# Kernel tuning notes

Hardware: AMD Instinct MI355X
Metric: run time of the kernel (lower is better)

The kernel has to match this reference:

```python
import jax, jax.numpy as jnp
import numpy as np

N_NODES = 50000
N_EDGES = 800000
D_IN = 128
D_HID = 128
D_OUT = 128


def _gcn_layer(x, W, b, src, dst, norm):
    # dense projection then edge-weighted gather -> scatter-add at dst
    h = x @ W                                   # [N, d_out]
    msg = h[src] * norm[:, None]                # [E, d_out]
    out = jax.ops.segment_sum(msg, dst, num_segments=N_NODES)
    return out + b


def setup_inputs() -> dict:
    key = jax.random.key(0)
    k = jax.random.split(key, 8)
    x = jax.random.normal(k[0], (N_NODES, D_IN), dtype=jnp.float32)
    edge_index = jax.random.randint(k[1], (2, N_EDGES), 0, N_NODES, dtype=jnp.int64)
    edge_weight = jax.random.uniform(k[2], (N_EDGES,), dtype=jnp.float32)
    # GCNConv params (glorot-ish scale)
    s1 = 1.0 / np.sqrt(D_IN)
    s2 = 1.0 / np.sqrt(D_HID)
    W1 = jax.random.normal(k[3], (D_IN, D_HID), dtype=jnp.float32) * s1
    b1 = jnp.zeros((D_HID,), dtype=jnp.float32)
    W2 = jax.random.normal(k[4], (D_HID, D_OUT), dtype=jnp.float32) * s2
    b2 = jnp.zeros((D_OUT,), dtype=jnp.float32)
    return {"x": x, "edge_index": edge_index, "edge_weight": edge_weight,
            "W1": W1, "b1": b1, "W2": W2, "b2": b2}


def reference(x, edge_index, edge_weight, W1, b1, W2, b2):
    src, dst = edge_index[0], edge_index[1]
    # gcn_norm (add_self_loops=False): deg from scatter-add of edge_weight at dst
    deg = jax.ops.segment_sum(edge_weight, dst, num_segments=N_NODES)
    dinv = jnp.where(deg > 0, jax.lax.rsqrt(jnp.maximum(deg, 1e-30)), 0.0)
    norm = dinv[src] * edge_weight * dinv[dst]  # [E]
    h = jax.nn.relu(_gcn_layer(x, W1, b1, src, dst, norm))
    out = _gcn_layer(h, W2, b2, src, dst, norm)
    # F.dropout in eval mode (deterministic reference) is identity
    return out
```

## Files before the change

kernel.cpp:

```cpp
#include <hip/hip_runtime.h>

#define N_NODES 50000
#define N_EDGES 800000
#define D 128
#define MAXDEG 64
#define NBUCK 196
#define BUCKCAP 5120
#define EPB 4096
#define NBB 196
#define GB 782
#define SP 136

typedef __attribute__((ext_vector_type(8))) short bf16x8;
typedef __attribute__((ext_vector_type(4))) float f32x4;

__device__ inline unsigned short f2bf(float f) {
    unsigned u = __float_as_uint(f);
    unsigned r = (u + 0x7fffu + ((u >> 16) & 1u)) >> 16;
    return (unsigned short)r;
}

__global__ __launch_bounds__(256) void k_bucket(const int* __restrict__ src,
                                                const int* __restrict__ dst,
                                                const float* __restrict__ ew,
                                                int* __restrict__ cursor,
                                                uint2* __restrict__ buck,
                                                const float* __restrict__ W1,
                                                const float* __restrict__ W2,
                                                unsigned short* __restrict__ Wt1,
                                                unsigned short* __restrict__ Wt2) {
    if (blockIdx.x >= NBB) {
        const float* W = (blockIdx.x == NBB) ? W1 : W2;
        unsigned short* Wt = (blockIdx.x == NBB) ? Wt1 : Wt2;
        for (int idx = threadIdx.x; idx < D * D; idx += 256) {
            int n = idx & 127, k = idx >> 7;
            Wt[n * D + k] = f2bf(W[k * D + n]);
        }
        return;
    }
    __shared__ uint2 sorted[EPB];
    __shared__ int hist[NBUCK];
    __shared__ int scn[NBUCK];
    __shared__ int gbase[NBUCK];
    __shared__ int s[256];
    int tid = threadIdx.x;
    int e0 = blockIdx.x * EPB;
    for (int i = tid; i < NBUCK; i += 256) hist[i] = 0;
    __syncthreads();
    #pragma unroll
    for (int j = 0; j < 16; ++j) {
        int e = e0 + j * 256 + tid;
        if (e < N_EDGES) atomicAdd(&hist[dst[e] >> 8], 1);
    }
    __syncthreads();
    int v = tid < NBUCK ? hist[tid] : 0;
    s[tid] = v;
    __syncthreads();
    for (int off = 1; off < 256; off <<= 1) {
        int u = tid >= off ? s[tid - off] : 0;
        __syncthreads();
        s[tid] += u;
        __syncthreads();
    }
    int excl = s[tid] - v;
    if (tid < NBUCK) {
        scn[tid] = excl;
        gbase[tid] = v ? atomicAdd(&cursor[tid], v) : 0;
        hist[tid] = excl;
    }
    __syncthreads();
    #pragma unroll
    for (int j = 0; j < 16; ++j) {
        int e = e0 + j * 256 + tid;
        if (e < N_EDGES) {
            int d = dst[e];
            int sv = src[e];
            unsigned wf = min(__float2uint_rn(ew[e] * 65536.f), 65535u);
            int slot = atomicAdd(&hist[d >> 8], 1);
            sorted[slot] = make_uint2(((unsigned)sv << 16) | wf, (unsigned)d);
        }
    }
    __syncthreads();
    int total = min(EPB, N_EDGES - e0);
    for (int i = tid; i < total; i += 256) {
        uint2 en = sorted[i];
        int bk = (int)(en.y >> 8);
        int g = gbase[bk] + (i - scn[bk]);
        if (g < BUCKCAP)
            buck[(size_t)bk * BUCKCAP + g] = make_uint2(en.x, en.y & 255u);
    }
}

__global__ __launch_bounds__(256) void k_build_gemm(
        const int* __restrict__ cursor, const uint2* __restrict__ buck,
        unsigned* __restrict__ csr, int* __restrict__ cnt,
        float* __restrict__ dinv,
        const float* __restrict__ X, const unsigned short* __restrict__ Wt1,
        unsigned short* __restrict__ h0) {
    __shared__ union SM {
        struct {
            unsigned csr_loc[256 * MAXDEG];
            int cnt_loc[256];
            int deg_loc[256];
        } b;
        unsigned short sX[64 * D];
    } sm;
    int tid = threadIdx.x;

    if (blockIdx.x < NBUCK) {
        int b = blockIdx.x;
        sm.b.cnt_loc[tid] = 0;
        sm.b.deg_loc[tid] = 0;
        {
            uint4* z4 = (uint4*)sm.b.csr_loc;
            #pragma unroll
            for (int i = 0; i < (256 * MAXDEG / 4) / 256; ++i)
                z4[i * 256 + tid] = make_uint4(0u, 0u, 0u, 0u);
        }
        __syncthreads();
        int n = min(cursor[b], BUCKCAP);
        const uint2* bb = buck + (size_t)b * BUCKCAP;
        for (int i = tid; i < n; i += 256) {
            uint2 e = bb[i];
            int ln = e.y;
            int slot = atomicAdd(&sm.b.cnt_loc[ln], 1);
            if (slot < MAXDEG) sm.b.csr_loc[ln * MAXDEG + slot] = e.x;
            atomicAdd(&sm.b.deg_loc[ln], (int)(e.x & 0xffffu));
        }
        __syncthreads();
        int node0 = b * 256;
        int nnodes = min(256, N_NODES - node0);
        uint4* g = (uint4*)(csr + (size_t)node0 * MAXDEG);
        const uint4* l = (const uint4*)sm.b.csr_loc;
        int nv = nnodes * (MAXDEG / 4);
        for (int i = tid; i < nv; i += 256) g[i] = l[i];
        if (tid < nnodes) {
            int node = node0 + tid;
            cnt[node] = min(sm.b.cnt_loc[tid], MAXDEG);
            float sum = (float)sm.b.deg_loc[tid] * (1.f / 65536.f);
            dinv[node] = sum > 0.f ? rsqrtf(fmaxf(sum, 1e-30f)) : 0.f;
        }
        return;
    }

    int row0 = (blockIdx.x - NBUCK) * 64;
    int nr = min(64, N_NODES - row0);
    {
        const float4* xs = (const float4*)(X + (size_t)row0 * D);
        int nvec = nr * (D / 4);
        for (int i = tid; i < nvec; i += 256) {
            float4 v = xs[i];
            ushort4 o;
            o.x = f2bf(v.x); o.y = f2bf(v.y); o.z = f2bf(v.z); o.w = f2bf(v.w);
            *(ushort4*)(sm.sX + i * 4) = o;
        }
    }
    __syncthreads();

    int wave = tid >> 6, lane = tid & 63;
    int m = lane & 15, quad = lane >> 4;
    f32x4 acc[8];
    #pragma unroll
    for (int i = 0; i < 8; ++i) acc[i] = (f32x4){0.f, 0.f, 0.f, 0.f};

    const unsigned short* aBase = sm.sX + (wave * 16 + m) * D + quad * 8;
    #pragma unroll
    for (int c = 0; c < 4; ++c) {
        bf16x8 a = *(const bf16x8*)(aBase + c * 32);
        #pragma unroll
        for (int n0 = 0; n0 < 8; ++n0) {
            bf16x8 b = *(const bf16x8*)(Wt1 + (n0 * 16 + m) * D + c * 32 + quad * 8);
            acc[n0] = __builtin_amdgcn_mfma_f32_16x16x32_bf16(a, b, acc[n0], 0, 0, 0);
        }
    }

    unsigned short* sOut = sm.sX + wave * 16 * D;
    __syncthreads();
    #pragma unroll
    for (int n0 = 0; n0 < 8; ++n0)
        #pragma unroll
        for (int i = 0; i < 4; ++i)
            sOut[(quad * 4 + i) * D + n0 * 16 + m] = f2bf(acc[n0][i]);
    __syncthreads();
    int rr = lane >> 2, c0 = (lane & 3) * 32;
    int grow = row0 + wave * 16 + rr;
    if (grow < N_NODES) {
        uint4* dstp = (uint4*)(h0 + (size_t)grow * D + c0);
        const uint4* srcp = (const uint4*)(sOut + rr * D + c0);
        dstp[0] = srcp[0]; dstp[1] = srcp[1]; dstp[2] = srcp[2]; dstp[3] = srcp[3];
    }
}

__global__ __launch_bounds__(256) void k_agg_mm(const unsigned short* __restrict__ H,
                                                const int* __restrict__ cnt,
                                                const unsigned* __restrict__ csr,
                                                const float* __restrict__ dinv,
                                                const float* __restrict__ b1,
                                                const unsigned short* __restrict__ Wt2,
                                                unsigned short* __restrict__ Hb) {
    __shared__ unsigned short sT[16 * SP];
    int tid = threadIdx.x, wave = tid >> 6, lane = tid & 63;
    int g = lane >> 4, fl = lane & 15;
    int nb = blockIdx.x * 16;
    int node = nb + wave * 4 + g;

    int end = min(cnt[node], MAXDEG);
    const uint4* row4 = (const uint4*)(csr + (size_t)node * MAXDEG);
    float acc[8] = {0.f, 0.f, 0.f, 0.f, 0.f, 0.f, 0.f, 0.f};
    for (int b0 = 0; b0 < end; b0 += 16) {
        int r0 = b0 >> 2;
        uint4 c0 = row4[r0], c1 = row4[r0 + 1], c2 = row4[r0 + 2], c3 = row4[r0 + 3];
        unsigned cs[16] = {c0.x, c0.y, c0.z, c0.w, c1.x, c1.y, c1.z, c1.w,
                           c2.x, c2.y, c2.z, c2.w, c3.x, c3.y, c3.z, c3.w};
        uint4 u[16];
        float nmv[16];
        #pragma unroll
        for (int j = 0; j < 16; ++j) {
            unsigned sv = cs[j] >> 16;
            u[j] = *(const uint4*)(H + (size_t)sv * D + fl * 8);
            nmv[j] = (float)(cs[j] & 0xffffu) * (1.f / 65536.f) * dinv[sv];
        }
        #pragma unroll
        for (int j = 0; j < 16; ++j) {
            unsigned a0[4] = {u[j].x, u[j].y, u[j].z, u[j].w};
            #pragma unroll
            for (int q = 0; q < 4; ++q) {
                acc[2 * q]     += __uint_as_float(a0[q] << 16) * nmv[j];
                acc[2 * q + 1] += __uint_as_float(a0[q] & 0xffff0000u) * nmv[j];
            }
        }
    }
    {
        float dn = dinv[node];
        int f = fl * 8;
        float4 bv0 = *(const float4*)(b1 + f);
        float4 bv1 = *(const float4*)(b1 + f + 4);
        ushort4 o0, o1;
        o0.x = f2bf(fmaxf(acc[0] * dn + bv0.x, 0.f));
        o0.y = f2bf(fmaxf(acc[1] * dn + bv0.y, 0.f));
        o0.z = f2bf(fmaxf(acc[2] * dn + bv0.z, 0.f));
        o0.w = f2bf(fmaxf(acc[3] * dn + bv0.w, 0.f));
        o1.x = f2bf(fmaxf(acc[4] * dn + bv1.x, 0.f));
        o1.y = f2bf(fmaxf(acc[5] * dn + bv1.y, 0.f));
        o1.z = f2bf(fmaxf(acc[6] * dn + bv1.z, 0.f));
        o1.w = f2bf(fmaxf(acc[7] * dn + bv1.w, 0.f));
        unsigned short* tp = sT + (wave * 4 + g) * SP + f;
        *(ushort4*)(tp) = o0;
        *(ushort4*)(tp + 4) = o1;
    }
    __syncthreads();

    int m = lane & 15, quad = lane >> 4;
    f32x4 acc2[2];
    acc2[0] = (f32x4){0.f, 0.f, 0.f, 0.f};
    acc2[1] = (f32x4){0.f, 0.f, 0.f, 0.f};
    #pragma unroll
    for (int c = 0; c < 4; ++c) {
        bf16x8 a = *(const bf16x8*)(sT + m * SP + c * 32 + quad * 8);
        #pragma unroll
        for (int t = 0; t < 2; ++t) {
            int n0 = wave * 2 + t;
            bf16x8 b = *(const bf16x8*)(Wt2 + (n0 * 16 + m) * D + c * 32 + quad * 8);
            acc2[t] = __builtin_amdgcn_mfma_f32_16x16x32_bf16(a, b, acc2[t], 0, 0, 0);
        }
    }
    float dv[4];
    #pragma unroll
    for (int i = 0; i < 4; ++i) dv[i] = dinv[nb + quad * 4 + i];
    __syncthreads();
    #pragma unroll
    for (int t = 0; t < 2; ++t)
        #pragma unroll
        for (int i = 0; i < 4; ++i)
            sT[(quad * 4 + i) * SP + (wave * 2 + t) * 16 + m] = f2bf(acc2[t][i] * dv[i]);
    __syncthreads();
    int rr = tid >> 4, cc = (tid & 15) * 8;
    *(uint4*)(Hb + (size_t)(nb + rr) * D + cc) = *(const uint4*)(sT + rr * SP + cc);
}

__global__ __launch_bounds__(256) void k_aggregate(const unsigned short* __restrict__ H,
                                                   const int* __restrict__ cnt,
                                                   const unsigned* __restrict__ csr,
                                                   const float* __restrict__ dinv,
                                                   const float* __restrict__ bias,
                                                   float* __restrict__ out) {
    int tid = threadIdx.x, wave = tid >> 6, lane = tid & 63;
    int g = lane >> 4, fl = lane & 15;
    int node = blockIdx.x * 16 + wave * 4 + g;

    int end = min(cnt[node], MAXDEG);
    const uint4* row4 = (const uint4*)(csr + (size_t)node * MAXDEG);
    float acc[8] = {0.f, 0.f, 0.f, 0.f, 0.f, 0.f, 0.f, 0.f};
    for (int b0 = 0; b0 < end; b0 += 16) {
        int r0 = b0 >> 2;
        uint4 c0 = row4[r0], c1 = row4[r0 + 1], c2 = row4[r0 + 2], c3 = row4[r0 + 3];
        unsigned cs[16] = {c0.x, c0.y, c0.z, c0.w, c1.x, c1.y, c1.z, c1.w,
                           c2.x, c2.y, c2.z, c2.w, c3.x, c3.y, c3.z, c3.w};
        uint4 u[16];
        float nmv[16];
        #pragma unroll
        for (int j = 0; j < 16; ++j) {
            unsigned sv = cs[j] >> 16;
            u[j] = *(const uint4*)(H + (size_t)sv * D + fl * 8);
            nmv[j] = (float)(cs[j] & 0xffffu) * (1.f / 65536.f);
        }
        #pragma unroll
        for (int j = 0; j < 16; ++j) {
            unsigned a0[4] = {u[j].x, u[j].y, u[j].z, u[j].w};
            #pragma unroll
            for (int q = 0; q < 4; ++q) {
                acc[2 * q]     += __uint_as_float(a0[q] << 16) * nmv[j];
                acc[2 * q + 1] += __uint_as_float(a0[q] & 0xffff0000u) * nmv[j];
            }
        }
    }
    float dn = dinv[node];
    int f = fl * 8;
    float4 bv0 = *(const float4*)(bias + f);
    float4 bv1 = *(const float4*)(bias + f + 4);
    float* op = out + (size_t)node * D + f;
    *(float4*)(op) = make_float4(acc[0] * dn + bv0.x, acc[1] * dn + bv0.y,
                                 acc[2] * dn + bv0.z, acc[3] * dn + bv0.w);
    *(float4*)(op + 4) = make_float4(acc[4] * dn + bv1.x, acc[5] * dn + bv1.y,
                                     acc[6] * dn + bv1.z, acc[7] * dn + bv1.w);
}

extern "C" void kernel_launch(void* const* d_in, const int* in_sizes, int n_in,
                              void* d_out, int out_size, void* d_ws, size_t ws_size,
                              hipStream_t stream) {
    const float* x   = (const float*)d_in[0];
    const int*   ei  = (const int*)d_in[1];
    const float* ew  = (const float*)d_in[2];
    const float* W1  = (const float*)d_in[3];
    const float* b1  = (const float*)d_in[4];
    const float* W2  = (const float*)d_in[5];
    const float* b2  = (const float*)d_in[6];
    float* out = (float*)d_out;

    const int* src = ei;
    const int* dst = ei + N_EDGES;

    char* base = (char*)d_ws;
    size_t off = 0;
    auto take = [&](size_t bytes) -> char* {
        char* p = base + off;
        off += (bytes + 255) & ~(size_t)255;
        return p;
    };
    int*      cursor = (int*)take(NBUCK * 4);
    size_t zero_bytes = off;
    float*    dinv = (float*)take(N_NODES * 4);
    int*      cnt  = (int*)take(N_NODES * 4);
    uint2*    buck = (uint2*)take((size_t)NBUCK * BUCKCAP * 8);
    unsigned* csr  = (unsigned*)take((size_t)N_NODES * MAXDEG * 4);
    unsigned short* Wt1 = (unsigned short*)take(D * D * 2);
    unsigned short* Wt2 = (unsigned short*)take(D * D * 2);
    unsigned short* h0  = (unsigned short*)take((size_t)N_NODES * D * 2);
    unsigned short* hb  = (unsigned short*)take((size_t)N_NODES * D * 2);

    hipMemsetAsync(d_ws, 0, zero_bytes, stream);

    const int FB = N_NODES / 16;

    k_bucket<<<NBB + 2, 256, 0, stream>>>(src, dst, ew, cursor, buck,
                                          W1, W2, Wt1, Wt2);
    k_build_gemm<<<NBUCK + GB, 256, 0, stream>>>(cursor, buck, csr, cnt, dinv,
                                                 x, Wt1, h0);
    k_agg_mm<<<FB, 256, 0, stream>>>(h0, cnt, csr, dinv, b1, Wt2, hb);
    k_aggregate<<<FB, 256, 0, stream>>>(hb, cnt, csr, dinv, b2, out);
}
```

Baseline: 196.9 us.

## Co-schedule edge bucket sort with first GEMM, split CSR build into own kernel

The weight transpose moves into a tiny separate kernel. The edge bucketing now runs in the same launch as the X·W1 GEMM blocks, and the CSR build becomes its own kernel. The GEMM used to share a launch with the CSR build; it now overlaps the sort instead. This rebalances the work so the large per-block LDS of the CSR build no longer sits with the GEMM blocks, at the cost of one extra kernel launch.

Result: slower. 212.6 us (+7.9%).

```diff
diff --git a/kernel.cpp b/kernel.cpp
--- a/kernel.cpp
+++ b/kernel.cpp
@@ -20,130 +20,87 @@
     return (unsigned short)r;
 }
 
-__global__ __launch_bounds__(256) void k_bucket(const int* __restrict__ src,
-                                                const int* __restrict__ dst,
-                                                const float* __restrict__ ew,
-                                                int* __restrict__ cursor,
-                                                uint2* __restrict__ buck,
-                                                const float* __restrict__ W1,
-                                                const float* __restrict__ W2,
-                                                unsigned short* __restrict__ Wt1,
-                                                unsigned short* __restrict__ Wt2) {
-    if (blockIdx.x >= NBB) {
-        const float* W = (blockIdx.x == NBB) ? W1 : W2;
-        unsigned short* Wt = (blockIdx.x == NBB) ? Wt1 : Wt2;
-        for (int idx = threadIdx.x; idx < D * D; idx += 256) {
-            int n = idx & 127, k = idx >> 7;
-            Wt[n * D + k] = f2bf(W[k * D + n]);
-        }
-        return;
-    }
-    __shared__ uint2 sorted[EPB];
-    __shared__ int hist[NBUCK];
-    __shared__ int scn[NBUCK];
-    __shared__ int gbase[NBUCK];
-    __shared__ int s[256];
-    int tid = threadIdx.x;
-    int e0 = blockIdx.x * EPB;
-    for (int i = tid; i < NBUCK; i += 256) hist[i] = 0;
-    __syncthreads();
-    #pragma unroll
-    for (int j = 0; j < 16; ++j) {
-        int e = e0 + j * 256 + tid;
-        if (e < N_EDGES) atomicAdd(&hist[dst[e] >> 8], 1);
-    }
-    __syncthreads();
-    int v = tid < NBUCK ? hist[tid] : 0;
-    s[tid] = v;
-    __syncthreads();
-    for (int off = 1; off < 256; off <<= 1) {
-        int u = tid >= off ? s[tid - off] : 0;
-        __syncthreads();
-        s[tid] += u;
-        __syncthreads();
-    }
-    int excl = s[tid] - v;
-    if (tid < NBUCK) {
-        scn[tid] = excl;
-        gbase[tid] = v ? atomicAdd(&cursor[tid], v) : 0;
-        hist[tid] = excl;
-    }
-    __syncthreads();
-    #pragma unroll
-    for (int j = 0; j < 16; ++j) {
-        int e = e0 + j * 256 + tid;
-        if (e < N_EDGES) {
-            int d = dst[e];
-            int sv = src[e];
-            unsigned wf = min(__float2uint_rn(ew[e] * 65536.f), 65535u);
-            int slot = atomicAdd(&hist[d >> 8], 1);
-            sorted[slot] = make_uint2(((unsigned)sv << 16) | wf, (unsigned)d);
-        }
-    }
-    __syncthreads();
-    int total = min(EPB, N_EDGES - e0);
-    for (int i = tid; i < total; i += 256) {
-        uint2 en = sorted[i];
-        int bk = (int)(en.y >> 8);
-        int g = gbase[bk] + (i - scn[bk]);
-        if (g < BUCKCAP)
-            buck[(size_t)bk * BUCKCAP + g] = make_uint2(en.x, en.y & 255u);
-    }
-}
-
-__global__ __launch_bounds__(256) void k_build_gemm(
-        const int* __restrict__ cursor, const uint2* __restrict__ buck,
-        unsigned* __restrict__ csr, int* __restrict__ cnt,
-        float* __restrict__ dinv,
+__global__ __launch_bounds__(256) void k_prep(const float* __restrict__ W1,
+                                              const float* __restrict__ W2,
+                                              unsigned short* __restrict__ Wt1,
+                                              unsigned short* __restrict__ Wt2) {
+    const float* W = (blockIdx.x == 0) ? W1 : W2;
+    unsigned short* Wt = (blockIdx.x == 0) ? Wt1 : Wt2;
+    for (int idx = threadIdx.x; idx < D * D; idx += 256) {
+        int n = idx & 127, k = idx >> 7;
+        Wt[n * D + k] = f2bf(W[k * D + n]);
+    }
+}
+
+__global__ __launch_bounds__(256) void k_sort_gemm(
+        const int* __restrict__ src, const int* __restrict__ dst,
+        const float* __restrict__ ew,
+        int* __restrict__ cursor, uint2* __restrict__ buck,
         const float* __restrict__ X, const unsigned short* __restrict__ Wt1,
         unsigned short* __restrict__ h0) {
     __shared__ union SM {
         struct {
-            unsigned csr_loc[256 * MAXDEG];
-            int cnt_loc[256];
-            int deg_loc[256];
-        } b;
+            uint2 sorted[EPB];
+            int hist[NBUCK];
+            int scn[NBUCK];
+            int gbase[NBUCK];
+            int s[256];
+        } so;
         unsigned short sX[64 * D];
     } sm;
     int tid = threadIdx.x;
 
-    if (blockIdx.x < NBUCK) {
-        int b = blockIdx.x;
-        sm.b.cnt_loc[tid] = 0;
-        sm.b.deg_loc[tid] = 0;
-        {
-            uint4* z4 = (uint4*)sm.b.csr_loc;
-            #pragma unroll
-            for (int i = 0; i < (256 * MAXDEG / 4) / 256; ++i)
-                z4[i * 256 + tid] = make_uint4(0u, 0u, 0u, 0u);
-        }
-        __syncthreads();
-        int n = min(cursor[b], BUCKCAP);
-        const uint2* bb = buck + (size_t)b * BUCKCAP;
-        for (int i = tid; i < n; i += 256) {
-            uint2 e = bb[i];
-            int ln = e.y;
-            int slot = atomicAdd(&sm.b.cnt_loc[ln], 1);
-            if (slot < MAXDEG) sm.b.csr_loc[ln * MAXDEG + slot] = e.x;
-            atomicAdd(&sm.b.deg_loc[ln], (int)(e.x & 0xffffu));
-        }
-        __syncthreads();
-        int node0 = b * 256;
-        int nnodes = min(256, N_NODES - node0);
-        uint4* g = (uint4*)(csr + (size_t)node0 * MAXDEG);
-        const uint4* l = (const uint4*)sm.b.csr_loc;
-        int nv = nnodes * (MAXDEG / 4);
-        for (int i = tid; i < nv; i += 256) g[i] = l[i];
-        if (tid < nnodes) {
-            int node = node0 + tid;
-            cnt[node] = min(sm.b.cnt_loc[tid], MAXDEG);
-            float sum = (float)sm.b.deg_loc[tid] * (1.f / 65536.f);
-            dinv[node] = sum > 0.f ? rsqrtf(fmaxf(sum, 1e-30f)) : 0.f;
+    if (blockIdx.x < NBB) {
+        int e0 = blockIdx.x * EPB;
+        for (int i = tid; i < NBUCK; i += 256) sm.so.hist[i] = 0;
+        __syncthreads();
+        #pragma unroll
+        for (int j = 0; j < 16; ++j) {
+            int e = e0 + j * 256 + tid;
+            if (e < N_EDGES) atomicAdd(&sm.so.hist[dst[e] >> 8], 1);
+        }
+        __syncthreads();
+        int v = tid < NBUCK ? sm.so.hist[tid] : 0;
+        sm.so.s[tid] = v;
+        __syncthreads();
+        for (int off = 1; off < 256; off <<= 1) {
+            int u = tid >= off ? sm.so.s[tid - off] : 0;
+            __syncthreads();
+            sm.so.s[tid] += u;
+            __syncthreads();
+        }
+        int excl = sm.so.s[tid] - v;
+        if (tid < NBUCK) {
+            sm.so.scn[tid] = excl;
+            sm.so.gbase[tid] = v ? atomicAdd(&cursor[tid], v) : 0;
+            sm.so.hist[tid] = excl;
+        }
+        __syncthreads();
+        #pragma unroll
+        for (int j = 0; j < 16; ++j) {
+            int e = e0 + j * 256 + tid;
+            if (e < N_EDGES) {
+                int d = dst[e];
+                int sv = src[e];
+                unsigned wf = min(__float2uint_rn(ew[e] * 65536.f), 65535u);
+                int slot = atomicAdd(&sm.so.hist[d >> 8], 1);
+                sm.so.sorted[slot] = make_uint2(((unsigned)sv << 16) | wf,
+                                                (unsigned)d);
+            }
+        }
+        __syncthreads();
+        int total = min(EPB, N_EDGES - e0);
+        for (int i = tid; i < total; i += 256) {
+            uint2 en = sm.so.sorted[i];
+            int bk = (int)(en.y >> 8);
+            int g = sm.so.gbase[bk] + (i - sm.so.scn[bk]);
+            if (g < BUCKCAP)
+                buck[(size_t)bk * BUCKCAP + g] = make_uint2(en.x, en.y & 255u);
         }
         return;
     }
 
-    int row0 = (blockIdx.x - NBUCK) * 64;
+    int row0 = (blockIdx.x - NBB) * 64;
     int nr = min(64, N_NODES - row0);
     {
         const float4* xs = (const float4*)(X + (size_t)row0 * D);
@@ -188,6 +145,48 @@
         uint4* dstp = (uint4*)(h0 + (size_t)grow * D + c0);
         const uint4* srcp = (const uint4*)(sOut + rr * D + c0);
         dstp[0] = srcp[0]; dstp[1] = srcp[1]; dstp[2] = srcp[2]; dstp[3] = srcp[3];
+    }
+}
+
+__global__ __launch_bounds__(256) void k_build(
+        const int* __restrict__ cursor, const uint2* __restrict__ buck,
+        unsigned* __restrict__ csr, int* __restrict__ cnt,
+        float* __restrict__ dinv) {
+    __shared__ unsigned csr_loc[256 * MAXDEG];
+    __shared__ int cnt_loc[256];
+    __shared__ int deg_loc[256];
+    int tid = threadIdx.x;
+    int b = blockIdx.x;
+    cnt_loc[tid] = 0;
+    deg_loc[tid] = 0;
+    {
+        uint4* z4 = (uint4*)csr_loc;
+        #pragma unroll
+        for (int i = 0; i < (256 * MAXDEG / 4) / 256; ++i)
+            z4[i * 256 + tid] = make_uint4(0u, 0u, 0u, 0u);
+    }
+    __syncthreads();
+    int n = min(cursor[b], BUCKCAP);
+    const uint2* bb = buck + (size_t)b * BUCKCAP;
+    for (int i = tid; i < n; i += 256) {
+        uint2 e = bb[i];
+        int ln = e.y;
+        int slot = atomicAdd(&cnt_loc[ln], 1);
+        if (slot < MAXDEG) csr_loc[ln * MAXDEG + slot] = e.x;
+        atomicAdd(&deg_loc[ln], (int)(e.x & 0xffffu));
+    }
+    __syncthreads();
+    int node0 = b * 256;
+    int nnodes = min(256, N_NODES - node0);
+    uint4* g = (uint4*)(csr + (size_t)node0 * MAXDEG);
+    const uint4* l = (const uint4*)csr_loc;
+    int nv = nnodes * (MAXDEG / 4);
+    for (int i = tid; i < nv; i += 256) g[i] = l[i];
+    if (tid < nnodes) {
+        int node = node0 + tid;
+        cnt[node] = min(cnt_loc[tid], MAXDEG);
+        float sum = (float)deg_loc[tid] * (1.f / 65536.f);
+        dinv[node] = sum > 0.f ? rsqrtf(fmaxf(sum, 1e-30f)) : 0.f;
     }
 }
 
@@ -362,10 +361,10 @@
 
     const int FB = N_NODES / 16;
 
-    k_bucket<<<NBB + 2, 256, 0, stream>>>(src, dst, ew, cursor, buck,
-                                          W1, W2, Wt1, Wt2);
-    k_build_gemm<<<NBUCK + GB, 256, 0, stream>>>(cursor, buck, csr, cnt, dinv,
-                                                 x, Wt1, h0);
+    k_prep<<<2, 256, 0, stream>>>(W1, W2, Wt1, Wt2);
+    k_sort_gemm<<<NBB + GB, 256, 0, stream>>>(src, dst, ew, cursor, buck,
+                                              x, Wt1, h0);
+    k_build<<<NBUCK, 256, 0, stream>>>(cursor, buck, csr, cnt, dinv);
     k_agg_mm<<<FB, 256, 0, stream>>>(h0, cnt, csr, dinv, b1, Wt2, hb);
     k_aggregate<<<FB, 256, 0, stream>>>(hb, cnt, csr, dinv, b2, out);
 }
```
